# Kernel tuning notes

Measured on AMD Instinct MI355X. Metric: run time of the kernel, lower is better.

## Reference

```python
import jax, jax.numpy as jnp
import numpy as np

N_SPECIES = 4
HIDDEN = 256
SILU_GAIN = 1.6765  # normalization constant for SiLU (1/sqrt(E[silu(x)^2]) for x~N(0,1))
AVG_N_ATOMS = 64.0  # average_number_of_atoms from the training set


def _norm_linear(x, w):
    # normalize_func('linear_no_bias', Linear): bias-free linear scaled by 1/sqrt(fan_in)
    return (x @ w) * (1.0 / np.sqrt(w.shape[0]))


def _norm_silu(x):
    # normalize_func('activation', SiLU): variance-preserving SiLU
    return jax.nn.silu(x) * SILU_GAIN


def _species_mlp(x, w1, w2, w3, w4):
    h = _norm_silu(_norm_linear(x, w1))
    h = _norm_silu(_norm_linear(h, w2))
    h = _norm_silu(_norm_linear(h, w3))
    return _norm_linear(h, w4)[:, 0]  # [n_atoms]


def setup_inputs() -> dict:
    key = jax.random.key(0)
    ks = jax.random.split(key, 8)
    n_atoms, n_feat, n_structures = 32768, 1920, 512
    features = jax.random.normal(ks[0], (n_atoms, n_feat), dtype=jnp.float32)
    species = jax.random.randint(ks[1], (n_atoms,), 0, N_SPECIES)
    structure_indices = jnp.sort(jax.random.randint(ks[2], (n_atoms,), 0, n_structures))
    W1 = jax.random.normal(ks[3], (N_SPECIES, n_feat, HIDDEN), dtype=jnp.float32)
    W2 = jax.random.normal(ks[4], (N_SPECIES, HIDDEN, HIDDEN), dtype=jnp.float32)
    W3 = jax.random.normal(ks[5], (N_SPECIES, HIDDEN, HIDDEN), dtype=jnp.float32)
    W4 = jax.random.normal(ks[6], (N_SPECIES, HIDDEN, 1), dtype=jnp.float32)
    composition_coefficients = jax.random.normal(ks[7], (N_SPECIES,), dtype=jnp.float32)
    return {
        "features": features,
        "W1": W1, "W2": W2, "W3": W3, "W4": W4,
        "composition_coefficients": composition_coefficients,
        "species": species,
        "structure_indices": structure_indices,
        "n_structures": n_structures,
    }


def reference(features, W1, W2, W3, W4, composition_coefficients,
              species, structure_indices, n_structures):
    # Per-species MLP heads (loop over the small, fixed species set; jit-friendly
    # replacement for ragged per-center_type gather blocks).
    per_species = jnp.stack(
        [_species_mlp(features, W1[s], W2[s], W3[s], W4[s]) for s in range(N_SPECIES)],
        axis=0,
    )  # [S, n_atoms]
    atomic_energies = jnp.take_along_axis(per_species, species[None, :], axis=0)[0]
    # energies.index_add_ over structure index
    energies = jax.ops.segment_sum(atomic_energies, structure_indices,
                                   num_segments=n_structures)
    energies = energies * (AVG_N_ATOMS ** -0.5)
    # composition term: per-structure species counts @ coefficients
    onehot = jax.nn.one_hot(species, N_SPECIES, dtype=features.dtype)
    comp = jax.ops.segment_sum(onehot, structure_indices, num_segments=n_structures)
    energies = energies + comp @ composition_coefficients
    return energies
```

## Files before the change

kernel.cpp:

```cpp
#include <hip/hip_runtime.h>

#define NATOMS 32768
#define NFEAT 1920
#define HIDDEN 256
#define NSPEC 4
#define NSTRUCT 512
#define BK 32
#define MT128 260
#define MPAD (MT128 * 128)
#define KC 960
#define NTL1 (KC / BK)
#define NBLK1 (MT128 * 2)
#define NBLK2 ((MPAD / 64) * 2)

typedef __bf16 bf16x8 __attribute__((ext_vector_type(8)));
typedef float f32x4 __attribute__((ext_vector_type(4)));
typedef float f4v __attribute__((ext_vector_type(4)));
typedef unsigned short us4 __attribute__((ext_vector_type(4)));
typedef unsigned short us8 __attribute__((ext_vector_type(8)));

#define WS_INTS 0
#define WS_PERM 256
#define WS_W1T (WS_PERM + MPAD * 4)
#define WS_W2T WS_W1T
#define WS_W3T (WS_W2T + NSPEC * HIDDEN * HIDDEN * 2)
#define WS_W4T (WS_W1T + NSPEC * HIDDEN * NFEAT * 2)
#define WS_H1  (WS_W4T + 4096)
#define WS_H2  (WS_H1 + (size_t)MPAD * HIDDEN * 2)
#define WS_HP0 (WS_H2 + (size_t)MPAD * HIDDEN * 2)
#define WS_HP1 (WS_HP0 + (size_t)MPAD * HIDDEN * 2)
#define WS_END (WS_HP1 + (size_t)MPAD * HIDDEN * 2)

__device__ __forceinline__ unsigned short f2bf(float f) {
  unsigned int u = __float_as_uint(f);
  u += 0x7fffu + ((u >> 16) & 1u);
  return (unsigned short)(u >> 16);
}
__device__ __forceinline__ float bf2f(unsigned short s) {
  return __uint_as_float(((unsigned int)s) << 16);
}
__device__ __forceinline__ float silu_n(float x) {
  return (x / (1.f + __expf(-x))) * 1.6765f;
}

__device__ __forceinline__ void gll16(const void* g, void* l) {
  __builtin_amdgcn_global_load_lds(
      (const __attribute__((address_space(1))) void*)g,
      (__attribute__((address_space(3))) void*)l, 16, 0, 0);
}


__global__ void k_init(int* ints, int* perm, float* out) {
  int i = blockIdx.x * blockDim.x + threadIdx.x;
  if (i < MPAD) perm[i] = -1;
  if (i < NSTRUCT) out[i] = 0.f;
  if (i < 8) ints[i] = 0;
  if (i >= 32 && i < 48) ((float*)ints)[i] = 0.f;
}

__global__ void k_count(const int* __restrict__ species, int* counts) {
  __shared__ int c[NSPEC];
  int tid = threadIdx.x;
  if (tid < NSPEC) c[tid] = 0;
  __syncthreads();
  int s = species[blockIdx.x * 256 + tid];
  int lane = tid & 63;
#pragma unroll
  for (int sp = 0; sp < NSPEC; ++sp) {
    unsigned long long m = __ballot(s == sp);
    if (lane == 0 && m) atomicAdd(&c[sp], __popcll(m));
  }
  __syncthreads();
  if (tid < NSPEC && c[tid]) atomicAdd(&counts[tid], c[tid]);
}

__global__ void k_offsets(int* ints) {
  int* counts = ints;
  int* cursors = ints + 4;
  int* off = ints + 8;
  off[0] = 0;
  for (int s = 0; s < NSPEC; ++s) {
    off[s + 1] = off[s] + ((counts[s] + 127) & ~127);
    cursors[s] = off[s];
  }
}

__global__ void k_scatter(const int* __restrict__ species, int* ints, int* perm) {
  __shared__ int cnt[4][NSPEC];
  __shared__ int base[NSPEC];
  int tid = threadIdx.x;
  int w = tid >> 6, lane = tid & 63;
  int i = blockIdx.x * 256 + tid;
  int s = species[i];
  unsigned long long m0 = __ballot(s == 0);
  unsigned long long m1 = __ballot(s == 1);
  unsigned long long m2 = __ballot(s == 2);
  unsigned long long m3 = __ballot(s == 3);
  if (lane == 0) {
    cnt[w][0] = __popcll(m0);
    cnt[w][1] = __popcll(m1);
    cnt[w][2] = __popcll(m2);
    cnt[w][3] = __popcll(m3);
  }
  __syncthreads();
  if (tid < NSPEC) {
    int t = cnt[0][tid] + cnt[1][tid] + cnt[2][tid] + cnt[3][tid];
    base[tid] = t ? atomicAdd(&ints[4 + tid], t) : 0;
  }
  __syncthreads();
  unsigned long long mm = (s == 0) ? m0 : (s == 1) ? m1 : (s == 2) ? m2 : m3;
  int pos = base[s] + __popcll(mm & ((1ull << lane) - 1ull));
#pragma unroll
  for (int ww = 0; ww < 4; ++ww)
    if (ww < w) pos += cnt[ww][s];
  perm[pos] = i;
}

__global__ void k_wtile(const float* __restrict__ src, unsigned short* __restrict__ dst,
                        int K, int N) {
  __shared__ unsigned short T[64][72];
  int ntN = N >> 6, ntK = K >> 6;
  int per = ntK * ntN;
  int b = blockIdx.x;
  int s = b / per, rem = b % per;
  int k0 = (rem / ntN) << 6;
  int n0 = (rem % ntN) << 6;
  int tid = threadIdx.x;
  int r = tid >> 2, cb = (tid & 3) << 4;
  const float* p = src + ((size_t)s * K + k0 + r) * N + n0 + cb;
#pragma unroll
  for (int j = 0; j < 16; j += 4) {
    f4v v = *(const f4v*)(p + j);
#pragma unroll
    for (int e = 0; e < 4; ++e) T[r][cb + j + e] = f2bf(v[e]);
  }
  __syncthreads();
  unsigned short* base = dst + (size_t)s * HIDDEN * K;
  int row_n = n0 + r;
#pragma unroll
  for (int g2 = 0; g2 < 2; ++g2) {
    int kl = cb + g2 * 8;
    int kg = k0 + kl;
    int t = kg >> 5;
    int kgl = (kg >> 3) & 3;
    int lanepos = ((row_n & 15) << 2) | (kgl ^ ((row_n >> 2) & 3));
    unsigned short v[8];
#pragma unroll
    for (int e = 0; e < 8; ++e) v[e] = T[kl + e][r];
    uint4 u;
    u.x = v[0] | ((unsigned)v[1] << 16);
    u.y = v[2] | ((unsigned)v[3] << 16);
    u.z = v[4] | ((unsigned)v[5] << 16);
    u.w = v[6] | ((unsigned)v[7] << 16);
    *(uint4*)(base + (size_t)t * 8192 + ((row_n >> 4) << 9) + lanepos * 8) = u;
  }
}

__global__ void k_w4(const float* __restrict__ src, unsigned short* __restrict__ dst) {
  int i = blockIdx.x * 256 + threadIdx.x;
  dst[i] = f2bf(src[i]);
}

__global__ __launch_bounds__(512) void k_l1(
    const float* __restrict__ xf, const unsigned short* __restrict__ Wt,
    unsigned short* __restrict__ Hp0, unsigned short* __restrict__ Hp1,
    const int* __restrict__ perm, const int* __restrict__ off,
    const float* __restrict__ zs, float scale) {
  __shared__ __align__(16) unsigned short Asl[2 * 8192];
  __shared__ __align__(16) unsigned short Bsl[2 * 8192];
  float* af = (float*)Asl;
  unsigned short* bl = Bsl;

  int nwg = gridDim.x;
  int xcd = blockIdx.x & 7, idx = blockIdx.x >> 3;
  int q = nwg >> 3, r = nwg & 7;
  int lb = (xcd < r ? xcd * (q + 1) : r * (q + 1) + (xcd - r) * q) + idx;
  int mt = lb >> 1, kc = lb & 1;

  int rowbase = mt * 128;
  int kbase = kc * KC;
  int tid = threadIdx.x;
  int w = tid >> 6, lane = tid & 63;
  int wr = w >> 2, wc = w & 3;

  int sp;
  if (rowbase < off[1]) sp = 0;
  else if (rowbase < off[2]) sp = 1;
  else if (rowbase < off[3]) sp = 2;
  else sp = 3;

  const unsigned short* wsp = Wt + (size_t)sp * HIDDEN * NFEAT + (size_t)(kc * NTL1) * 8192;
  const float* srcA[2];
  int ldsA[2];
#pragma unroll
  for (int qq = 0; qq < 2; ++qq) {
    int c = qq * 8 + w;
    int row = c * 8 + (lane >> 3);
    int slot = (lane & 7) ^ (row & 7);
    long as = perm[rowbase + row];
    srcA[qq] = (as >= 0) ? (xf + (size_t)as * NFEAT + kbase + slot * 4) : nullptr;
    ldsA[qq] = c * 256;
  }

  auto STAGE = [&](int b, int t) {
#pragma unroll
    for (int qq = 0; qq < 2; ++qq) {
      const float* s = srcA[qq] ? srcA[qq] + t * BK : zs;
      gll16(s, af + b * 4096 + ldsA[qq] + (lane & 63) * 4 - (lane & 63) * 4 + (lane * 4));
    }
#pragma unroll
    for (int qq = 0; qq < 2; ++qq)
      gll16(wsp + (size_t)t * 8192 + qq * 4096 + tid * 8, bl + b * 8192 + qq * 4096 + tid * 8);
  };

  f32x4 zero4 = {0.f, 0.f, 0.f, 0.f};
  f32x4 acc[4][4];
#pragma unroll
  for (int m = 0; m < 4; ++m)
#pragma unroll
    for (int n = 0; n < 4; ++n) acc[m][n] = zero4;

  int lr = lane & 15, lg = lane >> 4;

  STAGE(0, 0);
  __syncthreads();
  int buf = 0;
  for (int t = 0; t < NTL1; ++t) {
    if (t + 1 < NTL1) STAGE(buf ^ 1, t + 1);

    bf16x8 a[4], b[4];
#pragma unroll
    for (int m = 0; m < 4; ++m) {
      int row = wr * 64 + m * 16 + lr;
      const float* base = af + buf * 4096 + row * 32;
      f4v x0 = *(const f4v*)(base + (((lg << 1) ^ (row & 7)) << 2));
      f4v x1 = *(const f4v*)(base + ((((lg << 1) | 1) ^ (row & 7)) << 2));
      unsigned r01, r23, r45, r67;
      asm("v_cvt_pk_bf16_f32 %0, %1, %2" : "=v"(r01) : "v"(x0[0]), "v"(x0[1]));
      asm("v_cvt_pk_bf16_f32 %0, %1, %2" : "=v"(r23) : "v"(x0[2]), "v"(x0[3]));
      asm("v_cvt_pk_bf16_f32 %0, %1, %2" : "=v"(r45) : "v"(x1[0]), "v"(x1[1]));
      asm("v_cvt_pk_bf16_f32 %0, %1, %2" : "=v"(r67) : "v"(x1[2]), "v"(x1[3]));
      union { unsigned u[4]; bf16x8 v; } cv = {{r01, r23, r45, r67}};
      a[m] = cv.v;
    }
#pragma unroll
    for (int n = 0; n < 4; ++n) {
      int row = wc * 64 + n * 16 + lr;
      b[n] = *(const bf16x8*)(bl + buf * 8192 + row * 32 +
                              ((lg ^ ((row >> 2) & 3)) << 3));
    }
#pragma unroll
    for (int m = 0; m < 4; ++m)
#pragma unroll
      for (int n = 0; n < 4; ++n)
        acc[m][n] = __builtin_amdgcn_mfma_f32_16x16x32_bf16(a[m], b[n], acc[m][n], 0, 0, 0);

    __syncthreads();
    buf ^= 1;
  }

  unsigned short* Hp = kc ? Hp1 : Hp0;
#pragma unroll
  for (int m = 0; m < 4; ++m)
#pragma unroll
    for (int n = 0; n < 4; ++n)
#pragma unroll
      for (int rr = 0; rr < 4; ++rr)
        Hp[(size_t)(rowbase + wr * 64 + m * 16 + lg * 4 + rr) * HIDDEN +
           wc * 64 + n * 16 + lr] = f2bf(acc[m][n][rr] * scale);
}

__global__ __launch_bounds__(256) void k_mlp2s(
    const unsigned short* __restrict__ hp0, const unsigned short* __restrict__ hp1,
    const unsigned short* __restrict__ Wt, unsigned short* __restrict__ Hout,
    const int* __restrict__ off, float scale) {
  constexpr int K = HIDDEN;
  __shared__ __align__(16) unsigned short Asl[2 * 4096];
  __shared__ __align__(16) unsigned short Bsl[2 * 4096];
  unsigned short* ab = Asl;
  unsigned short* bl = Bsl;

  int nwg = gridDim.x;
  int xcd = blockIdx.x & 7, idx = blockIdx.x >> 3;
  int q = nwg >> 3, r = nwg & 7;
  int lb = (xcd < r ? xcd * (q + 1) : r * (q + 1) + (xcd - r) * q) + idx;
  int mt = lb >> 1, bn = lb & 1;

  int rowbase = mt * 64;
  int tid = threadIdx.x;
  int w = tid >> 6, lane = tid & 63;
  int wr = w >> 1, wc = w & 1;

  int sp;
  if (rowbase < off[1]) sp = 0;
  else if (rowbase < off[2]) sp = 1;
  else if (rowbase < off[3]) sp = 2;
  else sp = 3;

  const unsigned short* srcB[2];
  int ldsB[2];
#pragma unroll
  for (int qq = 0; qq < 2; ++qq) {
    int gc = bn * 8 + w * 2 + qq;
    srcB[qq] = Wt + (size_t)sp * HIDDEN * K + gc * 512 + lane * 8;
    ldsB[qq] = (w * 2 + qq) * 512;
  }
  int arow = w * 16 + (lane >> 2);
  int aslot = (lane & 3) ^ ((arow >> 2) & 3);
  const unsigned short* srcA0 = hp0 + ((size_t)(rowbase + arow)) * K + aslot * 8;
  const unsigned short* srcA1 = hp1 + ((size_t)(rowbase + arow)) * K + aslot * 8;
  int ldsA1 = w * 512;

  auto STAGE = [&](int b, int t) {
    gll16(srcA0 + t * BK, ab + b * 4096 + ldsA1);
    gll16(srcA1 + t * BK, ab + b * 4096 + 2048 + ldsA1);
#pragma unroll
    for (int qq = 0; qq < 2; ++qq)
      gll16(srcB[qq] + (size_t)t * 8192, bl + b * 4096 + ldsB[qq]);
  };

  f32x4 zero4 = {0.f, 0.f, 0.f, 0.f};
  f32x4 acc[2][4];
#pragma unroll
  for (int m = 0; m < 2; ++m)
#pragma unroll
    for (int n = 0; n < 4; ++n) acc[m][n] = zero4;

  int lr = lane & 15, lg = lane >> 4;
  constexpr int NT = K / BK;

  STAGE(0, 0);
  __syncthreads();
  int buf = 0;
  for (int t = 0; t < NT; ++t) {
    if (t + 1 < NT) STAGE(buf ^ 1, t + 1);

    bf16x8 a[2], b[4];
#pragma unroll
    for (int m = 0; m < 2; ++m) {
      int row = wr * 32 + m * 16 + lr;
      int o = buf * 4096 + row * 32 + ((lg ^ ((row >> 2) & 3)) << 3);
      us8 h0 = *(const us8*)(ab + o);
      us8 h1 = *(const us8*)(ab + 2048 + o);
      union { unsigned short u[8]; bf16x8 v; } cv;
#pragma unroll
      for (int e = 0; e < 8; ++e)
        cv.u[e] = f2bf(silu_n(bf2f(h0[e]) + bf2f(h1[e])));
      a[m] = cv.v;
    }
#pragma unroll
    for (int n = 0; n < 4; ++n) {
      int row = wc * 64 + n * 16 + lr;
      b[n] = *(const bf16x8*)(bl + buf * 4096 + row * 32 +
                              ((lg ^ ((row >> 2) & 3)) << 3));
    }
#pragma unroll
    for (int m = 0; m < 2; ++m)
#pragma unroll
      for (int n = 0; n < 4; ++n)
        acc[m][n] = __builtin_amdgcn_mfma_f32_16x16x32_bf16(a[m], b[n], acc[m][n], 0, 0, 0);

    __syncthreads();
    buf ^= 1;
  }

#pragma unroll
  for (int m = 0; m < 2; ++m)
#pragma unroll
    for (int n = 0; n < 4; ++n)
#pragma unroll
      for (int rr = 0; rr < 4; ++rr) {
        float v = acc[m][n][rr] * scale;
        Hout[(size_t)(rowbase + wr * 32 + m * 16 + lg * 4 + rr) * HIDDEN +
             bn * 128 + wc * 64 + n * 16 + lr] = f2bf(silu_n(v));
      }
}

__global__ __launch_bounds__(256) void k_mlp2(
    const unsigned short* __restrict__ xb, const unsigned short* __restrict__ Wt,
    unsigned short* __restrict__ Hout, const int* __restrict__ off, float scale) {
  constexpr int K = HIDDEN;
  __shared__ __align__(16) unsigned short Asl[2 * 2048];
  __shared__ __align__(16) unsigned short Bsl[2 * 4096];
  unsigned short* ab = Asl;
  unsigned short* bl = Bsl;

  int nwg = gridDim.x;
  int xcd = blockIdx.x & 7, idx = blockIdx.x >> 3;
  int q = nwg >> 3, r = nwg & 7;
  int lb = (xcd < r ? xcd * (q + 1) : r * (q + 1) + (xcd - r) * q) + idx;
  int mt = lb >> 1, bn = lb & 1;

  int rowbase = mt * 64;
  int tid = threadIdx.x;
  int w = tid >> 6, lane = tid & 63;
  int wr = w >> 1, wc = w & 1;

  int sp;
  if (rowbase < off[1]) sp = 0;
  else if (rowbase < off[2]) sp = 1;
  else if (rowbase < off[3]) sp = 2;
  else sp = 3;

  const unsigned short* srcB[2];
  int ldsB[2];
#pragma unroll
  for (int qq = 0; qq < 2; ++qq) {
    int gc = bn * 8 + w * 2 + qq;
    srcB[qq] = Wt + (size_t)sp * HIDDEN * K + gc * 512 + lane * 8;
    ldsB[qq] = (w * 2 + qq) * 512;
  }
  int arow = w * 16 + (lane >> 2);
  int aslot = (lane & 3) ^ ((arow >> 2) & 3);
  const unsigned short* srcA1 = xb + ((size_t)(rowbase + arow)) * K + aslot * 8;
  int ldsA1 = w * 512;

  auto STAGE = [&](int b, int t) {
    gll16(srcA1 + t * BK, ab + b * 2048 + ldsA1);
#pragma unroll
    for (int qq = 0; qq < 2; ++qq)
      gll16(srcB[qq] + (size_t)t * 8192, bl + b * 4096 + ldsB[qq]);
  };

  f32x4 zero4 = {0.f, 0.f, 0.f, 0.f};
  f32x4 acc[2][4];
#pragma unroll
  for (int m = 0; m < 2; ++m)
#pragma unroll
    for (int n = 0; n < 4; ++n) acc[m][n] = zero4;

  int lr = lane & 15, lg = lane >> 4;
  constexpr int NT = K / BK;

  STAGE(0, 0);
  __syncthreads();
  int buf = 0;
  for (int t = 0; t < NT; ++t) {
    if (t + 1 < NT) STAGE(buf ^ 1, t + 1);

    bf16x8 a[2], b[4];
#pragma unroll
    for (int m = 0; m < 2; ++m) {
      int row = wr * 32 + m * 16 + lr;
      a[m] = *(const bf16x8*)(ab + buf * 2048 + row * 32 +
                              ((lg ^ ((row >> 2) & 3)) << 3));
    }
#pragma unroll
    for (int n = 0; n < 4; ++n) {
      int row = wc * 64 + n * 16 + lr;
      b[n] = *(const bf16x8*)(bl + buf * 4096 + row * 32 +
                              ((lg ^ ((row >> 2) & 3)) << 3));
    }
#pragma unroll
    for (int m = 0; m < 2; ++m)
#pragma unroll
      for (int n = 0; n < 4; ++n)
        acc[m][n] = __builtin_amdgcn_mfma_f32_16x16x32_bf16(a[m], b[n], acc[m][n], 0, 0, 0);

    __syncthreads();
    buf ^= 1;
  }

#pragma unroll
  for (int m = 0; m < 2; ++m)
#pragma unroll
    for (int n = 0; n < 4; ++n)
#pragma unroll
      for (int rr = 0; rr < 4; ++rr) {
        float v = acc[m][n][rr] * scale;
        Hout[(size_t)(rowbase + wr * 32 + m * 16 + lg * 4 + rr) * HIDDEN +
             bn * 128 + wc * 64 + n * 16 + lr] = f2bf(silu_n(v));
      }
}

__global__ void k_l4(const unsigned short* __restrict__ H3, const unsigned short* __restrict__ W4t,
                     const int* __restrict__ perm, const int* __restrict__ species,
                     const int* __restrict__ sidx, const float* __restrict__ coeff,
                     float* __restrict__ out) {
  int w = threadIdx.x >> 6, l = threadIdx.x & 63;
  int row = blockIdx.x * 4 + w;
  int src = perm[row];
  if (src < 0) return;
  int sp = species[src];
  us4 h = *(const us4*)&H3[(size_t)row * HIDDEN + l * 4];
  us4 wv = *(const us4*)&W4t[sp * HIDDEN + l * 4];
  float sum = 0.f;
#pragma unroll
  for (int e = 0; e < 4; ++e) sum += bf2f(h[e]) * bf2f(wv[e]);
#pragma unroll
  for (int d = 32; d >= 1; d >>= 1) sum += __shfl_xor(sum, d, 64);
  if (l == 0)
    atomicAdd(&out[sidx[src]], sum * (0.0625f * 0.125f) + coeff[sp]);
}

extern "C" void kernel_launch(void* const* d_in, const int* in_sizes, int n_in,
                              void* d_out, int out_size, void* d_ws, size_t ws_size,
                              hipStream_t stream) {
  const float* features = (const float*)d_in[0];
  const float* W1 = (const float*)d_in[1];
  const float* W2 = (const float*)d_in[2];
  const float* W3 = (const float*)d_in[3];
  const float* W4 = (const float*)d_in[4];
  const float* coeff = (const float*)d_in[5];
  const int* species = (const int*)d_in[6];
  const int* sidx = (const int*)d_in[7];
  float* out = (float*)d_out;

  char* ws = (char*)d_ws;
  int* ints = (int*)(ws + WS_INTS);
  const float* zs = (const float*)(ws + 128);
  int* perm = (int*)(ws + WS_PERM);
  unsigned short* W1t = (unsigned short*)(ws + WS_W1T);
  unsigned short* W2t = (unsigned short*)(ws + WS_W2T);
  unsigned short* W3t = (unsigned short*)(ws + WS_W3T);
  unsigned short* W4t = (unsigned short*)(ws + WS_W4T);
  unsigned short* H1 = (unsigned short*)(ws + WS_H1);
  unsigned short* H2 = (unsigned short*)(ws + WS_H2);
  unsigned short* Hp0 = (unsigned short*)(ws + WS_HP0);
  unsigned short* Hp1 = (unsigned short*)(ws + WS_HP1);

  k_init<<<(MPAD + 255) / 256, 256, 0, stream>>>(ints, perm, out);
  k_count<<<NATOMS / 256, 256, 0, stream>>>(species, ints);
  k_offsets<<<1, 1, 0, stream>>>(ints);
  k_scatter<<<NATOMS / 256, 256, 0, stream>>>(species, ints, perm);

  k_wtile<<<NSPEC * (NFEAT / 64) * (HIDDEN / 64), 256, 0, stream>>>(W1, W1t, NFEAT, HIDDEN);
  k_w4<<<NSPEC, 256, 0, stream>>>(W4, W4t);

  const float s1 = 1.f / sqrtf((float)NFEAT);
  const float s2 = 1.f / 16.f;

  k_l1<<<NBLK1, 512, 0, stream>>>(features, W1t, Hp0, Hp1, perm, ints + 8, zs, s1);

  k_wtile<<<NSPEC * (HIDDEN / 64) * (HIDDEN / 64), 256, 0, stream>>>(W2, W2t, HIDDEN, HIDDEN);
  k_wtile<<<NSPEC * (HIDDEN / 64) * (HIDDEN / 64), 256, 0, stream>>>(W3, W3t, HIDDEN, HIDDEN);

  k_mlp2s<<<NBLK2, 256, 0, stream>>>(Hp0, Hp1, W2t, H2, ints + 8, s2);
  k_mlp2<<<NBLK2, 256, 0, stream>>>(H2, W3t, H1, ints + 8, s2);

  k_l4<<<MPAD / 4, 256, 0, stream>>>(H1, W4t, perm, species, sidx, coeff, out);
}
```

Before: 204.4 us.

## Load activations directly to registers, bypass LDS, shrink row tiles to 64

```diff
diff --git a/kernel.cpp b/kernel.cpp
--- a/kernel.cpp
+++ b/kernel.cpp
@@ -6,15 +6,16 @@
 #define NSPEC 4
 #define NSTRUCT 512
 #define BK 32
-#define MT128 260
-#define MPAD (MT128 * 128)
+#define MT 516
+#define MPAD (MT * 64)
 #define KC 960
-#define NTL1 (KC / BK)
-#define NBLK1 (MT128 * 2)
-#define NBLK2 ((MPAD / 64) * 2)
+#define NT1 (KC / BK)
+#define NBLK1 (MT * 2)
+#define NBLK2 (MT * 2)
 
 typedef __bf16 bf16x8 __attribute__((ext_vector_type(8)));
 typedef float f32x4 __attribute__((ext_vector_type(4)));
+typedef float f32x8v __attribute__((ext_vector_type(8)));
 typedef float f4v __attribute__((ext_vector_type(4)));
 typedef unsigned short us4 __attribute__((ext_vector_type(4)));
 typedef unsigned short us8 __attribute__((ext_vector_type(8)));
@@ -55,7 +56,6 @@
   if (i < MPAD) perm[i] = -1;
   if (i < NSTRUCT) out[i] = 0.f;
   if (i < 8) ints[i] = 0;
-  if (i >= 32 && i < 48) ((float*)ints)[i] = 0.f;
 }
 
 __global__ void k_count(const int* __restrict__ species, int* counts) {
@@ -80,7 +80,7 @@
   int* off = ints + 8;
   off[0] = 0;
   for (int s = 0; s < NSPEC; ++s) {
-    off[s + 1] = off[s] + ((counts[s] + 127) & ~127);
+    off[s + 1] = off[s] + ((counts[s] + 63) & ~63);
     cursors[s] = off[s];
   }
 }
@@ -161,14 +161,11 @@
   dst[i] = f2bf(src[i]);
 }
 
-__global__ __launch_bounds__(512) void k_l1(
+__global__ __launch_bounds__(256) void k_l1d(
     const float* __restrict__ xf, const unsigned short* __restrict__ Wt,
     unsigned short* __restrict__ Hp0, unsigned short* __restrict__ Hp1,
-    const int* __restrict__ perm, const int* __restrict__ off,
-    const float* __restrict__ zs, float scale) {
-  __shared__ __align__(16) unsigned short Asl[2 * 8192];
+    const int* __restrict__ perm, const int* __restrict__ off, float scale) {
   __shared__ __align__(16) unsigned short Bsl[2 * 8192];
-  float* af = (float*)Asl;
   unsigned short* bl = Bsl;
 
   int nwg = gridDim.x;
@@ -177,11 +174,11 @@
   int lb = (xcd < r ? xcd * (q + 1) : r * (q + 1) + (xcd - r) * q) + idx;
   int mt = lb >> 1, kc = lb & 1;
 
-  int rowbase = mt * 128;
+  int rowbase = mt * 64;
   int kbase = kc * KC;
   int tid = threadIdx.x;
-  int w = tid >> 6, lane = tid & 63;
-  int wr = w >> 2, wc = w & 3;
+  int wc = tid >> 6, lane = tid & 63;
+  int lr = lane & 15, lg = lane >> 4;
 
   int sp;
   if (rowbase < off[1]) sp = 0;
@@ -189,28 +186,21 @@
   else if (rowbase < off[3]) sp = 2;
   else sp = 3;
 
-  const unsigned short* wsp = Wt + (size_t)sp * HIDDEN * NFEAT + (size_t)(kc * NTL1) * 8192;
-  const float* srcA[2];
-  int ldsA[2];
-#pragma unroll
-  for (int qq = 0; qq < 2; ++qq) {
-    int c = qq * 8 + w;
-    int row = c * 8 + (lane >> 3);
-    int slot = (lane & 7) ^ (row & 7);
-    long as = perm[rowbase + row];
-    srcA[qq] = (as >= 0) ? (xf + (size_t)as * NFEAT + kbase + slot * 4) : nullptr;
-    ldsA[qq] = c * 256;
-  }
-
-  auto STAGE = [&](int b, int t) {
-#pragma unroll
-    for (int qq = 0; qq < 2; ++qq) {
-      const float* s = srcA[qq] ? srcA[qq] + t * BK : zs;
-      gll16(s, af + b * 4096 + ldsA[qq] + (lane & 63) * 4 - (lane & 63) * 4 + (lane * 4));
-    }
-#pragma unroll
-    for (int qq = 0; qq < 2; ++qq)
-      gll16(wsp + (size_t)t * 8192 + qq * 4096 + tid * 8, bl + b * 8192 + qq * 4096 + tid * 8);
+  const float* rp[4];
+  bool val[4];
+#pragma unroll
+  for (int m = 0; m < 4; ++m) {
+    long as = perm[rowbase + m * 16 + lr];
+    val[m] = (as >= 0);
+    rp[m] = xf + (val[m] ? (size_t)as * NFEAT : 0) + kbase + lg * 8;
+  }
+
+  const unsigned short* wsp = Wt + (size_t)sp * HIDDEN * NFEAT + (size_t)(kc * NT1) * 8192;
+  auto STAGEB = [&](int b, int t) {
+#pragma unroll
+    for (int qq = 0; qq < 4; ++qq)
+      gll16(wsp + (size_t)t * 8192 + qq * 2048 + tid * 8,
+            bl + b * 8192 + qq * 2048 + tid * 8);
   };
 
   f32x4 zero4 = {0.f, 0.f, 0.f, 0.f};
@@ -220,28 +210,28 @@
 #pragma unroll
     for (int n = 0; n < 4; ++n) acc[m][n] = zero4;
 
-  int lr = lane & 15, lg = lane >> 4;
-
-  STAGE(0, 0);
-  __syncthreads();
+  auto LOADF = [&](int t, f32x8v (&fr)[4]) {
+#pragma unroll
+    for (int m = 0; m < 4; ++m) fr[m] = *(const f32x8v*)(rp[m] + t * 32);
+  };
+
   int buf = 0;
-  for (int t = 0; t < NTL1; ++t) {
-    if (t + 1 < NTL1) STAGE(buf ^ 1, t + 1);
-
+  auto BODY = [&](int t, f32x8v (&cur)[4], f32x8v (&nxt)[4]) {
+    if (t + 1 < NT1) {
+      STAGEB(buf ^ 1, t + 1);
+      LOADF(t + 1, nxt);
+    }
     bf16x8 a[4], b[4];
 #pragma unroll
     for (int m = 0; m < 4; ++m) {
-      int row = wr * 64 + m * 16 + lr;
-      const float* base = af + buf * 4096 + row * 32;
-      f4v x0 = *(const f4v*)(base + (((lg << 1) ^ (row & 7)) << 2));
-      f4v x1 = *(const f4v*)(base + ((((lg << 1) | 1) ^ (row & 7)) << 2));
       unsigned r01, r23, r45, r67;
-      asm("v_cvt_pk_bf16_f32 %0, %1, %2" : "=v"(r01) : "v"(x0[0]), "v"(x0[1]));
-      asm("v_cvt_pk_bf16_f32 %0, %1, %2" : "=v"(r23) : "v"(x0[2]), "v"(x0[3]));
-      asm("v_cvt_pk_bf16_f32 %0, %1, %2" : "=v"(r45) : "v"(x1[0]), "v"(x1[1]));
-      asm("v_cvt_pk_bf16_f32 %0, %1, %2" : "=v"(r67) : "v"(x1[2]), "v"(x1[3]));
+      asm("v_cvt_pk_bf16_f32 %0, %1, %2" : "=v"(r01) : "v"(cur[m][0]), "v"(cur[m][1]));
+      asm("v_cvt_pk_bf16_f32 %0, %1, %2" : "=v"(r23) : "v"(cur[m][2]), "v"(cur[m][3]));
+      asm("v_cvt_pk_bf16_f32 %0, %1, %2" : "=v"(r45) : "v"(cur[m][4]), "v"(cur[m][5]));
+      asm("v_cvt_pk_bf16_f32 %0, %1, %2" : "=v"(r67) : "v"(cur[m][6]), "v"(cur[m][7]));
       union { unsigned u[4]; bf16x8 v; } cv = {{r01, r23, r45, r67}};
-      a[m] = cv.v;
+      union { unsigned u[4]; bf16x8 v; } zu = {{0, 0, 0, 0}};
+      a[m] = val[m] ? cv.v : zu.v;
     }
 #pragma unroll
     for (int n = 0; n < 4; ++n) {
@@ -254,9 +244,17 @@
 #pragma unroll
       for (int n = 0; n < 4; ++n)
         acc[m][n] = __builtin_amdgcn_mfma_f32_16x16x32_bf16(a[m], b[n], acc[m][n], 0, 0, 0);
-
     __syncthreads();
     buf ^= 1;
+  };
+
+  f32x8v fA[4], fB[4];
+  STAGEB(0, 0);
+  LOADF(0, fA);
+  __syncthreads();
+  for (int t2 = 0; t2 < NT1 / 2; ++t2) {
+    BODY(2 * t2, fA, fB);
+    BODY(2 * t2 + 1, fB, fA);
   }
 
   unsigned short* Hp = kc ? Hp1 : Hp0;
@@ -266,7 +264,7 @@
     for (int n = 0; n < 4; ++n)
 #pragma unroll
       for (int rr = 0; rr < 4; ++rr)
-        Hp[(size_t)(rowbase + wr * 64 + m * 16 + lg * 4 + rr) * HIDDEN +
+        Hp[(size_t)(rowbase + m * 16 + lg * 4 + rr) * HIDDEN +
            wc * 64 + n * 16 + lr] = f2bf(acc[m][n][rr] * scale);
 }
 
@@ -275,9 +273,7 @@
     const unsigned short* __restrict__ Wt, unsigned short* __restrict__ Hout,
     const int* __restrict__ off, float scale) {
   constexpr int K = HIDDEN;
-  __shared__ __align__(16) unsigned short Asl[2 * 4096];
   __shared__ __align__(16) unsigned short Bsl[2 * 4096];
-  unsigned short* ab = Asl;
   unsigned short* bl = Bsl;
 
   int nwg = gridDim.x;
@@ -290,6 +286,7 @@
   int tid = threadIdx.x;
   int w = tid >> 6, lane = tid & 63;
   int wr = w >> 1, wc = w & 1;
+  int lr = lane & 15, lg = lane >> 4;
 
   int sp;
   if (rowbase < off[1]) sp = 0;
@@ -305,15 +302,16 @@
     srcB[qq] = Wt + (size_t)sp * HIDDEN * K + gc * 512 + lane * 8;
     ldsB[qq] = (w * 2 + qq) * 512;
   }
-  int arow = w * 16 + (lane >> 2);
-  int aslot = (lane & 3) ^ ((arow >> 2) & 3);
-  const unsigned short* srcA0 = hp0 + ((size_t)(rowbase + arow)) * K + aslot * 8;
-  const unsigned short* srcA1 = hp1 + ((size_t)(rowbase + arow)) * K + aslot * 8;
-  int ldsA1 = w * 512;
+  const unsigned short* ra0[2];
+  const unsigned short* ra1[2];
+#pragma unroll
+  for (int m = 0; m < 2; ++m) {
+    size_t row = (size_t)(rowbase + wr * 32 + m * 16 + lr);
+    ra0[m] = hp0 + row * K + lg * 8;
+    ra1[m] = hp1 + row * K + lg * 8;
+  }
 
   auto STAGE = [&](int b, int t) {
-    gll16(srcA0 + t * BK, ab + b * 4096 + ldsA1);
-    gll16(srcA1 + t * BK, ab + b * 4096 + 2048 + ldsA1);
 #pragma unroll
     for (int qq = 0; qq < 2; ++qq)
       gll16(srcB[qq] + (size_t)t * 8192, bl + b * 4096 + ldsB[qq]);
@@ -326,9 +324,7 @@
 #pragma unroll
     for (int n = 0; n < 4; ++n) acc[m][n] = zero4;
 
-  int lr = lane & 15, lg = lane >> 4;
   constexpr int NT = K / BK;
-
   STAGE(0, 0);
   __syncthreads();
   int buf = 0;
@@ -338,10 +334,8 @@
     bf16x8 a[2], b[4];
 #pragma unroll
     for (int m = 0; m < 2; ++m) {
-      int row = wr * 32 + m * 16 + lr;
-      int o = buf * 4096 + row * 32 + ((lg ^ ((row >> 2) & 3)) << 3);
-      us8 h0 = *(const us8*)(ab + o);
-      us8 h1 = *(const us8*)(ab + 2048 + o);
+      us8 h0 = *(const us8*)(ra0[m] + t * BK);
+      us8 h1 = *(const us8*)(ra1[m] + t * BK);
       union { unsigned short u[8]; bf16x8 v; } cv;
 #pragma unroll
       for (int e = 0; e < 8; ++e)
@@ -376,13 +370,11 @@
       }
 }
 
-__global__ __launch_bounds__(256) void k_mlp2(
+__global__ __launch_bounds__(256) void k_mlp3(
     const unsigned short* __restrict__ xb, const unsigned short* __restrict__ Wt,
     unsigned short* __restrict__ Hout, const int* __restrict__ off, float scale) {
   constexpr int K = HIDDEN;
-  __shared__ __align__(16) unsigned short Asl[2 * 2048];
   __shared__ __align__(16) unsigned short Bsl[2 * 4096];
-  unsigned short* ab = Asl;
   unsigned short* bl = Bsl;
 
   int nwg = gridDim.x;
@@ -395,6 +387,7 @@
   int tid = threadIdx.x;
   int w = tid >> 6, lane = tid & 63;
   int wr = w >> 1, wc = w & 1;
+  int lr = lane & 15, lg = lane >> 4;
 
   int sp;
   if (rowbase < off[1]) sp = 0;
@@ -410,13 +403,14 @@
     srcB[qq] = Wt + (size_t)sp * HIDDEN * K + gc * 512 + lane * 8;
     ldsB[qq] = (w * 2 + qq) * 512;
   }
-  int arow = w * 16 + (lane >> 2);
-  int aslot = (lane & 3) ^ ((arow >> 2) & 3);
-  const unsigned short* srcA1 = xb + ((size_t)(rowbase + arow)) * K + aslot * 8;
-  int ldsA1 = w * 512;
+  const unsigned short* ra[2];
+#pragma unroll
+  for (int m = 0; m < 2; ++m) {
+    size_t row = (size_t)(rowbase + wr * 32 + m * 16 + lr);
+    ra[m] = xb + row * K + lg * 8;
+  }
 
   auto STAGE = [&](int b, int t) {
-    gll16(srcA1 + t * BK, ab + b * 2048 + ldsA1);
 #pragma unroll
     for (int qq = 0; qq < 2; ++qq)
       gll16(srcB[qq] + (size_t)t * 8192, bl + b * 4096 + ldsB[qq]);
@@ -429,9 +423,7 @@
 #pragma unroll
     for (int n = 0; n < 4; ++n) acc[m][n] = zero4;
 
-  int lr = lane & 15, lg = lane >> 4;
   constexpr int NT = K / BK;
-
   STAGE(0, 0);
   __syncthreads();
   int buf = 0;
@@ -440,11 +432,8 @@
 
     bf16x8 a[2], b[4];
 #pragma unroll
-    for (int m = 0; m < 2; ++m) {
-      int row = wr * 32 + m * 16 + lr;
-      a[m] = *(const bf16x8*)(ab + buf * 2048 + row * 32 +
-                              ((lg ^ ((row >> 2) & 3)) << 3));
-    }
+    for (int m = 0; m < 2; ++m)
+      a[m] = *(const bf16x8*)(ra[m] + t * BK);
 #pragma unroll
     for (int n = 0; n < 4; ++n) {
       int row = wc * 64 + n * 16 + lr;
@@ -508,7 +497,6 @@
 
   char* ws = (char*)d_ws;
   int* ints = (int*)(ws + WS_INTS);
-  const float* zs = (const float*)(ws + 128);
   int* perm = (int*)(ws + WS_PERM);
   unsigned short* W1t = (unsigned short*)(ws + WS_W1T);
   unsigned short* W2t = (unsigned short*)(ws + WS_W2T);
@@ -530,13 +518,13 @@
   const float s1 = 1.f / sqrtf((float)NFEAT);
   const float s2 = 1.f / 16.f;
 
-  k_l1<<<NBLK1, 512, 0, stream>>>(features, W1t, Hp0, Hp1, perm, ints + 8, zs, s1);
+  k_l1d<<<NBLK1, 256, 0, stream>>>(features, W1t, Hp0, Hp1, perm, ints + 8, s1);
 
   k_wtile<<<NSPEC * (HIDDEN / 64) * (HIDDEN / 64), 256, 0, stream>>>(W2, W2t, HIDDEN, HIDDEN);
   k_wtile<<<NSPEC * (HIDDEN / 64) * (HIDDEN / 64), 256, 0, stream>>>(W3, W3t, HIDDEN, HIDDEN);
 
   k_mlp2s<<<NBLK2, 256, 0, stream>>>(Hp0, Hp1, W2t, H2, ints + 8, s2);
-  k_mlp2<<<NBLK2, 256, 0, stream>>>(H2, W3t, H1, ints + 8, s2);
+  k_mlp3<<<NBLK2, 256, 0, stream>>>(H2, W3t, H1, ints + 8, s2);
 
   k_l4<<<MPAD / 4, 256, 0, stream>>>(H1, W4t, perm, species, sidx, coeff, out);
 }
```

After: 306.0 us. +49.7%, slower.
